# Kernel optimization log

Hardware: AMD Instinct MI355X
Metric: run time of the kernel (lower is better)

The kernel has to match this reference:

```python
import jax, jax.numpy as jnp
import numpy as np

L = 1
K = 32
TEMP = 0.1
EPS = 1e-8  # torch cosine_similarity eps
D, N, DIM = 64, 8192, 256


def setup_inputs() -> dict:
    key = jax.random.key(0)
    embeddings = jax.random.normal(key, (D, N, DIM), dtype=jnp.float32)
    P = D - L
    rng = np.random.default_rng(0)
    sel = np.stack([
        rng.choice(np.delete(np.arange(2 * D), [i, i + L]), size=K, replace=False)
        for i in range(P)
    ])  # [P, K] negatives, excluding i and j, sampled w/o replacement
    return {"embeddings": embeddings, "neg_idx": jnp.asarray(sel, dtype=jnp.int32)}


def reference(embeddings, neg_idx):
    Dn, Nn, d = embeddings.shape
    # per-item sum and hard-negative sum (drop top-K by L2 norm)
    sum_all = embeddings.sum(axis=1)                      # [D, d]
    norms = jnp.linalg.norm(embeddings, axis=2)           # [D, N]
    top_idx = jnp.argsort(-norms, axis=1)[:, :K]          # [D, K]
    top_sum = jnp.take_along_axis(embeddings, top_idx[:, :, None], axis=1).sum(axis=1)
    sum_neg = sum_all - top_sum                           # == sum of masked rows
    samples = jnp.concatenate([sum_all, sum_neg], axis=0)  # [2D, d]
    nS = samples / jnp.maximum(jnp.linalg.norm(samples, axis=1, keepdims=True), EPS)

    P = Dn - L
    ii = jnp.arange(P)
    jj = ii + L
    nS_sg = jax.lax.stop_gradient(nS)  # s_j is detached in positive sims
    pos = jnp.sum(nS[ii] * nS_sg[jj], axis=-1)            # [P] (== pos_sim_ij == pos_sim_ji)
    negs = nS[neg_idx]                                    # [P, K, d]
    neg_i = jnp.einsum('pd,pkd->pk', nS[ii], negs)
    neg_j = jnp.einsum('pd,pkd->pk', nS[jj], negs)

    def nce(pos_s, neg_s):
        logits = jnp.concatenate([pos_s[:, None], neg_s], axis=1) / TEMP
        return -(pos_s / TEMP - jax.scipy.special.logsumexp(logits, axis=1))

    total = jnp.sum(nce(pos, neg_i) + nce(pos, neg_j)) / (2.0 * P)
    return total
```

## Files before the change

kernel.cpp:

```cpp
#include <hip/hip_runtime.h>
#include <math.h>

constexpr int D_ = 64;
constexpr int N_ = 8192;
constexpr int DIM_ = 256;
constexpr int K_ = 32;
constexpr int L_ = 1;
constexpr int P_ = D_ - L_;
constexpr float TEMP_ = 0.1f;
constexpr float EPS_ = 1e-8f;

constexpr int CHUNKS = 32;
constexpr int CROWS = 256;
constexpr int BATCH = 16;
constexpr int LDSTR = 65;

typedef float f32x4 __attribute__((ext_vector_type(4)));

__global__ __launch_bounds__(256, 4) void k1_sums_norms(const float* __restrict__ emb,
                                                        float* __restrict__ normsq,
                                                        float* __restrict__ psum) {
  const int b = blockIdx.x;
  const int d = b >> 5;
  const int chunk = b & 31;
  const int tid = threadIdx.x;
  const int wave = tid >> 6;
  const int lane = tid & 63;
  const float* base = emb + (size_t)d * N_ * DIM_;

  __shared__ __align__(16) float sq[4][BATCH * LDSTR];

  float a0 = 0.f, a1 = 0.f, a2 = 0.f, a3 = 0.f;

  for (int batch = 0; batch < 4; ++batch) {
    const int brow0 = chunk * CROWS + batch * 64;
#pragma unroll
    for (int r = 0; r < BATCH; ++r) {
      const int grow = brow0 + (r << 2) + wave;
      const f32x4 v = __builtin_nontemporal_load(
          reinterpret_cast<const f32x4*>(base + (size_t)grow * DIM_ + (lane << 2)));
      a0 += v.x; a1 += v.y; a2 += v.z; a3 += v.w;
      sq[wave][r * LDSTR + lane] = v.x * v.x + v.y * v.y + v.z * v.z + v.w * v.w;
    }
    {
      const int rr = tid >> 2;
      const int q = tid & 3;
      const int r = rr & 15;
      const float* p = &sq[wave][r * LDSTR + q * 16];
      float s = 0.f;
#pragma unroll
      for (int i = 0; i < 16; ++i) s += p[i];
      s += __shfl_xor(s, 1, 64);
      s += __shfl_xor(s, 2, 64);
      if (q == 0) {
        const int row = brow0 + (r << 2) + wave;
        normsq[(size_t)d * N_ + row] = s;
      }
    }
  }

  reinterpret_cast<float4*>(&sq[wave][0])[lane] = make_float4(a0, a1, a2, a3);
  __syncthreads();
  const float s = sq[0][tid] + sq[1][tid] + sq[2][tid] + sq[3][tid];
  psum[(size_t)(d * CHUNKS + chunk) * DIM_ + tid] = s;
}

__global__ __launch_bounds__(256) void k23_topk_samples(const float* __restrict__ emb,
                                                        const float* __restrict__ normsq,
                                                        const float* __restrict__ psum,
                                                        float* __restrict__ nS,
                                                        float* __restrict__ out) {
  const int d = blockIdx.x;
  const int tid = threadIdx.x;
  const int lane = tid & 63;
  const int wave = tid >> 6;

  __shared__ float vals[N_];
  __shared__ unsigned long long wbest[4];
  __shared__ int topidx[K_];

  for (int i = tid; i < N_; i += 256) vals[i] = normsq[(size_t)d * N_ + i];

  float s1 = 0.f;
#pragma unroll 8
  for (int c = 0; c < CHUNKS; ++c)
    s1 += psum[(size_t)(d * CHUNKS + c) * DIM_ + tid];

  __syncthreads();

  unsigned long long my = 0ull;
#pragma unroll 8
  for (int r = 0; r < 32; ++r) {
    const int i = tid + (r << 8);
    const unsigned long long key =
        ((unsigned long long)__float_as_uint(vals[i]) << 32) | (unsigned)(N_ - 1 - i);
    if (key > my) my = key;
  }

  for (int k = 0; k < K_; ++k) {
    unsigned long long bw = my;
#pragma unroll
    for (int off = 1; off < 64; off <<= 1) {
      const unsigned long long o = __shfl_xor(bw, off, 64);
      if (o > bw) bw = o;
    }
    if (lane == 0) wbest[wave] = bw;
    __syncthreads();
    unsigned long long bb = wbest[0];
    for (int w = 1; w < 4; ++w)
      if (wbest[w] > bb) bb = wbest[w];
    const int idx = N_ - 1 - (int)(bb & 0xFFFFFFFFu);
    if (tid == 0) topidx[k] = idx;
    if ((idx & 255) == tid) {
      vals[idx] = 0.0f;
      my = 0ull;
      for (int r = 0; r < 32; ++r) {
        const int i = tid + (r << 8);
        const unsigned long long key =
            ((unsigned long long)__float_as_uint(vals[i]) << 32) | (unsigned)(N_ - 1 - i);
        if (key > my) my = key;
      }
    }
    __syncthreads();
  }

  const float* base = emb + (size_t)d * N_ * DIM_;
  float ts = 0.f;
#pragma unroll 4
  for (int k = 0; k < K_; ++k) {
    ts += base[(size_t)topidx[k] * DIM_ + tid];
  }
  const float s2 = s1 - ts;

  float q1 = s1 * s1, q2 = s2 * s2;
#pragma unroll
  for (int off = 32; off > 0; off >>= 1) {
    q1 += __shfl_down(q1, off, 64);
    q2 += __shfl_down(q2, off, 64);
  }
  __shared__ float w1[4], w2[4];
  __shared__ float inv1s, inv2s;
  if (lane == 0) { w1[wave] = q1; w2[wave] = q2; }
  __syncthreads();
  if (tid == 0) {
    const float n1 = sqrtf(w1[0] + w1[1] + w1[2] + w1[3]);
    const float n2 = sqrtf(w2[0] + w2[1] + w2[2] + w2[3]);
    inv1s = 1.0f / fmaxf(n1, EPS_);
    inv2s = 1.0f / fmaxf(n2, EPS_);
    if (d == 0) out[0] = 0.0f;
  }
  __syncthreads();
  nS[d * DIM_ + tid] = s1 * inv1s;
  nS[(D_ + d) * DIM_ + tid] = s2 * inv2s;
}

__global__ __launch_bounds__(256) void k4_loss(const float* __restrict__ nS,
                                               const int* __restrict__ negidx,
                                               float* __restrict__ out) {
  const int p = blockIdx.x;
  const int tid = threadIdx.x;
  const int wave = tid >> 6;
  const int lane = tid & 63;

  const float4 vi = *reinterpret_cast<const float4*>(nS + p * DIM_ + (lane << 2));
  const float4 vj = *reinterpret_cast<const float4*>(nS + (p + L_) * DIM_ + (lane << 2));

  float dp = vi.x * vj.x + vi.y * vj.y + vi.z * vj.z + vi.w * vj.w;
#pragma unroll
  for (int off = 1; off < 64; off <<= 1) dp += __shfl_xor(dp, off, 64);
  const float invT = 1.0f / TEMP_;
  const float posT = dp * invT;

  float mi = -INFINITY, si = 0.f, mj = -INFINITY, sj = 0.f;
#pragma unroll
  for (int kk = 0; kk < K_ / 4; ++kk) {
    const int k = wave * (K_ / 4) + kk;
    const int idx = negidx[p * K_ + k];
    const float4 vn = *reinterpret_cast<const float4*>(nS + idx * DIM_ + (lane << 2));
    float di = vi.x * vn.x + vi.y * vn.y + vi.z * vn.z + vi.w * vn.w;
    float dj = vj.x * vn.x + vj.y * vn.y + vj.z * vn.z + vj.w * vn.w;
#pragma unroll
    for (int off = 1; off < 64; off <<= 1) {
      di += __shfl_xor(di, off, 64);
      dj += __shfl_xor(dj, off, 64);
    }
    const float li = di * invT;
    const float lj = dj * invT;
    if (li > mi) { si = si * expf(mi - li) + 1.f; mi = li; } else { si += expf(li - mi); }
    if (lj > mj) { sj = sj * expf(mj - lj) + 1.f; mj = lj; } else { sj += expf(lj - mj); }
  }

  __shared__ float pm[2][4], ps[2][4];
  if (lane == 0) {
    pm[0][wave] = mi; ps[0][wave] = si;
    pm[1][wave] = mj; ps[1][wave] = sj;
  }
  __syncthreads();
  if (tid == 0) {
    float total = 0.f;
#pragma unroll
    for (int side = 0; side < 2; ++side) {
      float m = posT;
      for (int w = 0; w < 4; ++w) m = fmaxf(m, pm[side][w]);
      float s = expf(posT - m);
      for (int w = 0; w < 4; ++w) s += ps[side][w] * expf(pm[side][w] - m);
      total += m + logf(s) - posT;
    }
    atomicAdd(out, total / (2.0f * P_));
  }
}

extern "C" void kernel_launch(void* const* d_in, const int* in_sizes, int n_in,
                              void* d_out, int out_size, void* d_ws, size_t ws_size,
                              hipStream_t stream) {
  const float* emb = (const float*)d_in[0];
  const int* negidx = (const int*)d_in[1];
  float* out = (float*)d_out;

  float* normsq = (float*)d_ws;
  float* psum = normsq + (size_t)D_ * N_;
  float* nS = psum + (size_t)D_ * CHUNKS * DIM_;

  k1_sums_norms<<<D_ * CHUNKS, 256, 0, stream>>>(emb, normsq, psum);
  k23_topk_samples<<<D_, 256, 0, stream>>>(emb, normsq, psum, nS, out);
  k4_loss<<<P_, 256, 0, stream>>>(nS, negidx, out);
}
```

Before: 127.5 us.

## Replace iterative top-K argmax with threshold filter and bitonic sort

The 32-round serial block-wide argmax in the top-K stage is replaced. Each thread's max key is bitonic-sorted to find the 32nd-largest per-thread max, which serves as a threshold. Candidates at or above it are compacted into shared memory and sorted once more to pick the top 32. The old iterative path is kept as a fallback if more than 256 candidates qualify. This is meant to cut the many barriers and rescans per item, at the cost of two 256-element bitonic sorts with their own barriers.

```diff
diff --git a/kernel.cpp b/kernel.cpp
--- a/kernel.cpp
+++ b/kernel.cpp
@@ -14,7 +14,9 @@
 constexpr int CROWS = 256;
 constexpr int BATCH = 16;
 constexpr int LDSTR = 65;
-
+constexpr int CAP = 256;
+
+typedef unsigned long long u64;
 typedef float f32x4 __attribute__((ext_vector_type(4)));
 
 __global__ __launch_bounds__(256, 4) void k1_sums_norms(const float* __restrict__ emb,
@@ -65,6 +67,21 @@
   psum[(size_t)(d * CHUNKS + chunk) * DIM_ + tid] = s;
 }
 
+__device__ __forceinline__ void bitonic256_desc(u64* a, int tid) {
+  for (int size = 2; size <= 256; size <<= 1) {
+    for (int stride = size >> 1; stride > 0; stride >>= 1) {
+      __syncthreads();
+      const int partner = tid ^ stride;
+      if (partner > tid) {
+        const u64 x = a[tid], y = a[partner];
+        const bool desc = ((tid & size) == 0);
+        if (desc ? (x < y) : (x > y)) { a[tid] = y; a[partner] = x; }
+      }
+    }
+  }
+  __syncthreads();
+}
+
 __global__ __launch_bounds__(256) void k23_topk_samples(const float* __restrict__ emb,
                                                         const float* __restrict__ normsq,
                                                         const float* __restrict__ psum,
@@ -76,8 +93,10 @@
   const int wave = tid >> 6;
 
   __shared__ float vals[N_];
-  __shared__ unsigned long long wbest[4];
+  __shared__ u64 work[CAP];
+  __shared__ int cnt;
   __shared__ int topidx[K_];
+  __shared__ u64 wbest[4];
 
   for (int i = tid; i < N_; i += 256) vals[i] = normsq[(size_t)d * N_ + i];
 
@@ -88,40 +107,71 @@
 
   __syncthreads();
 
-  unsigned long long my = 0ull;
+  auto keyat = [&](int i) -> u64 {
+    return ((u64)__float_as_uint(vals[i]) << 32) | (unsigned)(N_ - 1 - i);
+  };
+
+  u64 my = 0ull;
 #pragma unroll 8
   for (int r = 0; r < 32; ++r) {
-    const int i = tid + (r << 8);
-    const unsigned long long key =
-        ((unsigned long long)__float_as_uint(vals[i]) << 32) | (unsigned)(N_ - 1 - i);
+    const u64 key = keyat(tid + (r << 8));
     if (key > my) my = key;
   }
-
-  for (int k = 0; k < K_; ++k) {
-    unsigned long long bw = my;
-#pragma unroll
-    for (int off = 1; off < 64; off <<= 1) {
-      const unsigned long long o = __shfl_xor(bw, off, 64);
-      if (o > bw) bw = o;
-    }
-    if (lane == 0) wbest[wave] = bw;
+  work[tid] = my;
+  __syncthreads();
+  bitonic256_desc(work, tid);
+  const u64 T = work[31];
+  __syncthreads();
+
+  if (tid == 0) cnt = 0;
+  __syncthreads();
+#pragma unroll 8
+  for (int r = 0; r < 32; ++r) {
+    const u64 key = keyat(tid + (r << 8));
+    if (key >= T) {
+      const int p = atomicAdd(&cnt, 1);
+      if (p < CAP) work[p] = key;
+    }
+  }
+  __syncthreads();
+  const int c = cnt;
+  if (c <= CAP) {
+    if (tid >= c) work[tid] = 0ull;
     __syncthreads();
-    unsigned long long bb = wbest[0];
-    for (int w = 1; w < 4; ++w)
-      if (wbest[w] > bb) bb = wbest[w];
-    const int idx = N_ - 1 - (int)(bb & 0xFFFFFFFFu);
-    if (tid == 0) topidx[k] = idx;
-    if ((idx & 255) == tid) {
-      vals[idx] = 0.0f;
-      my = 0ull;
-      for (int r = 0; r < 32; ++r) {
-        const int i = tid + (r << 8);
-        const unsigned long long key =
-            ((unsigned long long)__float_as_uint(vals[i]) << 32) | (unsigned)(N_ - 1 - i);
-        if (key > my) my = key;
-      }
-    }
+    bitonic256_desc(work, tid);
+    if (tid < K_) topidx[tid] = N_ - 1 - (int)(work[tid] & 0xFFFFFFFFull);
     __syncthreads();
+  } else {
+    __syncthreads();
+    u64 m2 = 0ull;
+    for (int r = 0; r < 32; ++r) {
+      const u64 key = keyat(tid + (r << 8));
+      if (key > m2) m2 = key;
+    }
+    for (int k = 0; k < K_; ++k) {
+      u64 bw = m2;
+#pragma unroll
+      for (int off = 1; off < 64; off <<= 1) {
+        const u64 o = __shfl_xor(bw, off, 64);
+        if (o > bw) bw = o;
+      }
+      if (lane == 0) wbest[wave] = bw;
+      __syncthreads();
+      u64 bb = wbest[0];
+      for (int w = 1; w < 4; ++w)
+        if (wbest[w] > bb) bb = wbest[w];
+      const int idx = N_ - 1 - (int)(bb & 0xFFFFFFFFull);
+      if (tid == 0) topidx[k] = idx;
+      if ((idx & 255) == tid) {
+        vals[idx] = 0.0f;
+        m2 = 0ull;
+        for (int r = 0; r < 32; ++r) {
+          const u64 key = keyat(tid + (r << 8));
+          if (key > m2) m2 = key;
+        }
+      }
+      __syncthreads();
+    }
   }
 
   const float* base = emb + (size_t)d * N_ * DIM_;
```

Result: faster. 111.1 us (-12.9%).
